# Performance work log

Hardware: AMD Instinct MI355X
Metric: run time of the kernel (lower is better)

Reference implementation:

```python
import jax, jax.numpy as jnp
import numpy as np

B = 16384          # batch_size
NF = 50            # n_fields
K = 16             # embedding_dim
V = 1_000_000      # input_dim (vocab)
H = 400            # fc hidden
NNZ = B * NF


def _xavier(key, shape):
    fan_in, fan_out = shape
    lim = (6.0 / (fan_in + fan_out)) ** 0.5
    return jax.random.uniform(key, shape, minval=-lim, maxval=lim, dtype=jnp.float32)


def setup_inputs() -> dict:
    key = jax.random.key(0)
    ks = jax.random.split(key, 12)
    feats = jax.random.randint(ks[0], (NNZ,), 0, V)
    # n_fields contiguous features per sample (required by view(batch_size,-1))
    index = jnp.repeat(jnp.arange(B), NF)
    values = jax.random.uniform(ks[1], (NNZ,), dtype=jnp.float32)
    bias = jnp.zeros((1, 1), jnp.float32)
    weights = _xavier(ks[2], (V, 1))
    embedding = _xavier(ks[3], (V, K))
    d = NF * K  # 800
    W0 = _xavier(ks[4], (d, H))
    b0 = jax.random.normal(ks[5], (1, 1), jnp.float32)
    W1 = _xavier(ks[6], (H, H))
    b1 = jax.random.normal(ks[7], (1, 1), jnp.float32)
    W2 = _xavier(ks[8], (H, 1))
    b2 = jax.random.normal(ks[9], (1, 1), jnp.float32)
    return dict(index=index, feats=feats, values=values, bias=bias,
                weights=weights, embedding=embedding,
                W0=W0, b0=b0, W1=W1, b1=b1, W2=W2, b2=b2, batch_size=B)


def reference(index, feats, values, bias, weights, embedding,
              W0, b0, W1, b1, W2, b2, batch_size):
    # gather (F.embedding)
    w = weights[feats, 0]              # [nnz]
    emb = embedding[feats]             # [nnz, K]

    # first order: segment-sum of w*v, plus bias ([B] + [1,1] -> [1,B], as in torch)
    first = jax.ops.segment_sum(w * values, index, num_segments=batch_size) + bias

    # second order: FM pooling trick, fused over all K dims in one segment reduce
    ev = emb * values[:, None]                                        # [nnz, K]
    s1 = jax.ops.segment_sum(ev, index, num_segments=batch_size)      # [B, K]
    s2 = jax.ops.segment_sum(ev * ev, index, num_segments=batch_size) # [B, K]
    second = 0.5 * jnp.sum(s1 * s1 - s2, axis=1)                      # [B]

    # higher order MLP (relu on every layer, scalar biases)
    x = emb.reshape(batch_size, -1)    # [B, NF*K]
    x = jax.nn.relu(x @ W0 + b0)
    x = jax.nn.relu(x @ W1 + b1)
    x = jax.nn.relu(x @ W2 + b2)       # [B, 1]
    higher = x.reshape(-1)             # [B]

    return jax.nn.sigmoid(first + second + higher)  # [1, B]
```

## Files before the change

### kernel.cpp

```cpp
#include <hip/hip_runtime.h>
#include <hip/hip_bf16.h>


#define BATCH 16384
#define NFLD  50
#define EK    16
#define DDIM  800
#define HDIM  400
#define HPAD  416
#define NPAD  512

#define TB_W0 400
#define TB_W1 208
#define TBLK  (TB_W0 + TB_W1)
#define GBLK  (BATCH / 16)

#define MROWS 64
#define NCOLS 448
#define WCOLS 112
#define NFRAG 7
#define P1    (DDIM / 32)
#define P2    (HPAD / 32)
#define H0S   424
#define NCHUNK (NCOLS / 16)

typedef __attribute__((ext_vector_type(8))) __bf16 bf16x8;
typedef __attribute__((ext_vector_type(4))) float  f32x4;

typedef const __attribute__((address_space(1))) unsigned int* gas_u32p;
typedef __attribute__((address_space(3))) unsigned int*       las_u32p;

__device__ __forceinline__ void gld_lds16(const void* g, void* l) {
    __builtin_amdgcn_global_load_lds((gas_u32p)g, (las_u32p)l, 16, 0, 0);
}

__global__ __launch_bounds__(256) void prep_kernel(
    const float* __restrict__ W0, const float* __restrict__ W1,
    __hip_bfloat16* __restrict__ W0t, __hip_bfloat16* __restrict__ W1t,
    const int* __restrict__ feats, const float* __restrict__ values,
    const float* __restrict__ biasp, const float* __restrict__ weights,
    const float* __restrict__ embedding,
    float* __restrict__ fs, __hip_bfloat16* __restrict__ x)
{
    const int bid = blockIdx.x;
    if (bid < TBLK) {
        const int which = bid >= TB_W0;
        const int i  = which ? bid - TB_W0 : bid;
        const int nx = which ? 13 : 25;
        const int bx = i % nx, by = i / nx;
        const float* src = which ? W1 : W0;
        __hip_bfloat16* dst = which ? W1t : W0t;
        const int srcK = which ? HDIM : DDIM;
        const int dstCols = which ? HPAD : DDIM;

        __shared__ float tile[32][33];
        const int tx = threadIdx.x & 31, ty = threadIdx.x >> 5;
        const int k0 = bx * 32, n0 = by * 32;
#pragma unroll
        for (int r = 0; r < 4; ++r) {
            int k = k0 + ty + r * 8;
            int n = n0 + tx;
            float v = (k < srcK && n < HDIM) ? src[(long)k * HDIM + n] : 0.f;
            tile[ty + r * 8][tx] = v;
        }
        __syncthreads();
#pragma unroll
        for (int r = 0; r < 4; ++r) {
            int n = n0 + ty + r * 8;
            int k = k0 + tx;
            if (k < dstCols)
                dst[(long)n * dstCols + k] = __float2bfloat16(tile[tx][ty + r * 8]);
        }
        return;
    }

    const int wave = threadIdx.x >> 6;
    const int lane = threadIdx.x & 63;
    const int r    = lane >> 2, c = lane & 3;
    const int sbase = (bid - TBLK) * 16 + wave * 4;

    int   f[4] = {0, 0, 0, 0};
    float v[4] = {0.f, 0.f, 0.f, 0.f};
    float wsum[4] = {0.f, 0.f, 0.f, 0.f};
#pragma unroll
    for (int q = 0; q < 4; ++q) {
        const long base = (long)(sbase + q) * NFLD;
        if (lane < NFLD) {
            f[q] = feats[base + lane];
            v[q] = values[base + lane];
            wsum[q] = weights[f[q]] * v[q];
        }
    }

    int   fj[4][4]; float vj[4][4];
#pragma unroll
    for (int q = 0; q < 4; ++q)
#pragma unroll
        for (int p = 0; p < 4; ++p) {
            const int j = p * 16 + r;
            if (p < 3 || r < 2) {
                fj[q][p] = __shfl(f[q], j);
                vj[q][p] = __shfl(v[q], j);
            }
        }
    float4 e[4][4];
#pragma unroll
    for (int q = 0; q < 4; ++q)
#pragma unroll
        for (int p = 0; p < 4; ++p)
            if (p < 3 || r < 2)
                e[q][p] = *(const float4*)(embedding + (long)fj[q][p] * EK + c * 4);

#pragma unroll
    for (int q = 0; q < 4; ++q) {
        const int s = sbase + q;
        f32x4 s1 = {0.f, 0.f, 0.f, 0.f}, s2 = {0.f, 0.f, 0.f, 0.f};
#pragma unroll
        for (int p = 0; p < 4; ++p) {
            const int j = p * 16 + r;
            if (p < 3 || r < 2) {
                f32x4 ef = {e[q][p].x, e[q][p].y, e[q][p].z, e[q][p].w};
                f32x4 ev = ef * vj[q][p];
                s1 += ev;
                s2 += ev * ev;
                __hip_bfloat16 pk[4] = {
                    __float2bfloat16(e[q][p].x), __float2bfloat16(e[q][p].y),
                    __float2bfloat16(e[q][p].z), __float2bfloat16(e[q][p].w)};
                *(uint2*)&x[(long)s * DDIM + j * EK + c * 4] = *(uint2*)pk;
            }
        }
#pragma unroll
        for (int m = 4; m <= 32; m <<= 1) {
            s1.x += __shfl_xor(s1.x, m); s1.y += __shfl_xor(s1.y, m);
            s1.z += __shfl_xor(s1.z, m); s1.w += __shfl_xor(s1.w, m);
            s2.x += __shfl_xor(s2.x, m); s2.y += __shfl_xor(s2.y, m);
            s2.z += __shfl_xor(s2.z, m); s2.w += __shfl_xor(s2.w, m);
        }
        float t = (s1.x * s1.x - s2.x) + (s1.y * s1.y - s2.y)
                + (s1.z * s1.z - s2.z) + (s1.w * s1.w - s2.w);
        t += __shfl_xor(t, 1); t += __shfl_xor(t, 2);
        float w = wsum[q];
        w += __shfl_xor(w, 1);  w += __shfl_xor(w, 2);
        w += __shfl_xor(w, 4);  w += __shfl_xor(w, 8);
        w += __shfl_xor(w, 16); w += __shfl_xor(w, 32);
        if (lane == 0) fs[s] = w + 0.5f * t + biasp[0];
    }
}

__global__ __launch_bounds__(512, 2) void fused_mlp_kernel(
    const __hip_bfloat16* __restrict__ x,
    const __hip_bfloat16* __restrict__ W0t, const __hip_bfloat16* __restrict__ W1t,
    const float* __restrict__ b0p, const float* __restrict__ b1p,
    const float* __restrict__ W2, const float* __restrict__ b2p,
    const float* __restrict__ fs, float* __restrict__ out)
{
    __shared__ __align__(16) __hip_bfloat16 sA[2][MROWS * 32];
    __shared__ __align__(16) __hip_bfloat16 sB[2][NCOLS * 32];
    __shared__ __align__(16) __hip_bfloat16 h0p[MROWS * H0S];
    __shared__ float red[MROWS][4];

    const int tid  = threadIdx.x;
    const int wave = tid >> 6, lane = tid & 63;
    const int l16  = lane & 15, quad = lane >> 4;
    const int waveM = wave & 1, waveN = wave >> 1;
    const int m0 = blockIdx.x * MROWS;
    const int rlane = lane >> 2, clane = (lane & 3) * 8;

    const float b0 = b0p[0];
    const float b1 = b1p[0];

    auto stage1 = [&](int p, int h) {
        const int k0 = p * 32;
#pragma unroll
        for (int c = 0; c < 4; ++c) {
            const int idx = wave * 4 + c;
            if (idx < 4) {
                gld_lds16(x + (long)(m0 + idx * 16 + rlane) * DDIM + k0 + clane,
                          &sA[h][idx * 512 + lane * 8]);
            } else {
                const int ch = idx - 4;
                gld_lds16(W0t + (long)(ch * 16 + rlane) * DDIM + k0 + clane,
                          &sB[h][ch * 512 + lane * 8]);
            }
        }
    };
    auto stage2 = [&](int p, int h) {
        const int k0 = p * 32;
#pragma unroll
        for (int c = 0; c < 4; ++c) {
            const int ch = wave + c * 8;
            if (ch < NCHUNK) {
                gld_lds16(W1t + (long)(ch * 16 + rlane) * HPAD + k0 + clane,
                          &sB[h][ch * 512 + lane * 8]);
            }
        }
    };

    f32x4 acc[2][NFRAG] = {};
    auto compute1 = [&](int h) {
        bf16x8 af[2], bfr[NFRAG];
#pragma unroll
        for (int i = 0; i < 2; ++i)
            af[i] = *(const bf16x8*)&sA[h][(waveM * 32 + i * 16 + l16) * 32 + quad * 8];
#pragma unroll
        for (int j = 0; j < NFRAG; ++j)
            bfr[j] = *(const bf16x8*)&sB[h][(waveN * WCOLS + j * 16 + l16) * 32 + quad * 8];
#pragma unroll
        for (int i = 0; i < 2; ++i)
#pragma unroll
            for (int j = 0; j < NFRAG; ++j)
                acc[i][j] = __builtin_amdgcn_mfma_f32_16x16x32_bf16(
                    af[i], bfr[j], acc[i][j], 0, 0, 0);
    };

    for (int kt = 0; kt + 1 < P1; kt += 2) {
        stage1(kt, 0); stage1(kt + 1, 1);
        __syncthreads();
        compute1(0); compute1(1);
        __syncthreads();
    }
    stage1(P1 - 1, 0);
    __syncthreads();
    compute1(0);
    __syncthreads();

#pragma unroll
    for (int i = 0; i < 2; ++i)
#pragma unroll
        for (int j = 0; j < NFRAG; ++j) {
            const int col = waveN * WCOLS + j * 16 + l16;
            if (col < HPAD) {
#pragma unroll
                for (int r = 0; r < 4; ++r) {
                    const int row = waveM * 32 + i * 16 + quad * 4 + r;
                    float v = acc[i][j][r] + b0;
                    v = v > 0.f ? v : 0.f;
                    if (col >= HDIM) v = 0.f;
                    h0p[row * H0S + col] = __float2bfloat16(v);
                }
            }
        }

    f32x4 acc2[2][NFRAG] = {};
    float w2v[NFRAG];
#pragma unroll
    for (int j = 0; j < NFRAG; ++j) {
        const int col = waveN * WCOLS + j * 16 + l16;
        w2v[j] = (col < HDIM) ? W2[col] : 0.f;
    }
    auto compute2 = [&](int h, int p) {
        bf16x8 af[2], bfr[NFRAG];
#pragma unroll
        for (int i = 0; i < 2; ++i)
            af[i] = *(const bf16x8*)&h0p[(waveM * 32 + i * 16 + l16) * H0S + p * 32 + quad * 8];
#pragma unroll
        for (int j = 0; j < NFRAG; ++j)
            bfr[j] = *(const bf16x8*)&sB[h][(waveN * WCOLS + j * 16 + l16) * 32 + quad * 8];
#pragma unroll
        for (int i = 0; i < 2; ++i)
#pragma unroll
            for (int j = 0; j < NFRAG; ++j)
                acc2[i][j] = __builtin_amdgcn_mfma_f32_16x16x32_bf16(
                    af[i], bfr[j], acc2[i][j], 0, 0, 0);
    };

    for (int kt = 0; kt + 1 < P2; kt += 2) {
        stage2(kt, 0); stage2(kt + 1, 1);
        __syncthreads();
        compute2(0, kt); compute2(1, kt + 1);
        __syncthreads();
    }
    stage2(P2 - 1, 0);
    __syncthreads();
    compute2(0, P2 - 1);

#pragma unroll
    for (int i = 0; i < 2; ++i)
#pragma unroll
        for (int r = 0; r < 4; ++r) {
            float ps = 0.f;
#pragma unroll
            for (int j = 0; j < NFRAG; ++j) {
                float v = acc2[i][j][r] + b1;
                v = v > 0.f ? v : 0.f;
                ps += v * w2v[j];
            }
            ps += __shfl_xor(ps, 1); ps += __shfl_xor(ps, 2);
            ps += __shfl_xor(ps, 4); ps += __shfl_xor(ps, 8);
            if (l16 == 0)
                red[waveM * 32 + i * 16 + quad * 4 + r][waveN] = ps;
        }
    __syncthreads();

    if (tid < MROWS) {
        const float s = (red[tid][0] + red[tid][1]) + (red[tid][2] + red[tid][3]);
        float hv = s + b2p[0];
        hv = hv > 0.f ? hv : 0.f;
        const float z = fs[m0 + tid] + hv;
        out[m0 + tid] = 1.f / (1.f + __expf(-z));
    }
}

extern "C" void kernel_launch(void* const* d_in, const int* in_sizes, int n_in,
                              void* d_out, int out_size, void* d_ws, size_t ws_size,
                              hipStream_t stream)
{
    const int*   feats     = (const int*)d_in[1];
    const float* values    = (const float*)d_in[2];
    const float* bias      = (const float*)d_in[3];
    const float* weights   = (const float*)d_in[4];
    const float* embedding = (const float*)d_in[5];
    const float* W0 = (const float*)d_in[6];
    const float* b0 = (const float*)d_in[7];
    const float* W1 = (const float*)d_in[8];
    const float* b1 = (const float*)d_in[9];
    const float* W2 = (const float*)d_in[10];
    const float* b2 = (const float*)d_in[11];

    char* ws = (char*)d_ws;
    size_t off = 0;
    auto alloc = [&](size_t bytes) {
        void* p = ws + off;
        off += (bytes + 255) & ~(size_t)255;
        return p;
    };
    float*          fs   = (float*)alloc((size_t)BATCH * 4);
    __hip_bfloat16* x    = (__hip_bfloat16*)alloc((size_t)BATCH * DDIM * 2);
    __hip_bfloat16* W0t  = (__hip_bfloat16*)alloc((size_t)NPAD * DDIM * 2);
    __hip_bfloat16* W1t  = (__hip_bfloat16*)alloc((size_t)NPAD * HPAD * 2);
    (void)ws_size; (void)in_sizes; (void)n_in; (void)out_size;

    prep_kernel<<<dim3(TBLK + GBLK), 256, 0, stream>>>(
        W0, W1, W0t, W1t, feats, values, bias, weights, embedding, fs, x);
    fused_mlp_kernel<<<dim3(BATCH / MROWS), 512, 0, stream>>>(
        x, W0t, W1t, b0, b1, W2, b2, fs, (float*)d_out);
}
```

Measured before the change: 181.1 us.

## Triple-buffer MLP GEMM staging with vmcnt waits, XOR swizzle and setprio

Replaces the double-buffered stage/compute loops of both MLP GEMMs with a three-stage ring buffer. Loads for step p+2 are issued before computing step p, and partial s_waitcnt vmcnt counts let the next loads stay in flight. The LDS tile layout gains an XOR swizzle on the K-chunk index to cut bank conflicts on fragment reads, and MFMA sections get raised wave priority. Because the LDS footprint grows, occupancy at two blocks per CU could suffer, and the hand-written vmcnt counts must exactly match the number of loads issued per wave.

```diff
diff --git a/kernel.cpp b/kernel.cpp
--- a/kernel.cpp
+++ b/kernel.cpp
@@ -22,7 +22,10 @@
 #define P1    (DDIM / 32)
 #define P2    (HPAD / 32)
 #define H0S   424
-#define NCHUNK (NCOLS / 16)
+#define SBUF  16384
+#define SBUF2 14336
+
+#define VMCNT(N) asm volatile("s_waitcnt vmcnt(" #N ")" ::: "memory")
 
 typedef __attribute__((ext_vector_type(8))) __bf16 bf16x8;
 typedef __attribute__((ext_vector_type(4))) float  f32x4;
@@ -32,6 +35,12 @@
 
 __device__ __forceinline__ void gld_lds16(const void* g, void* l) {
     __builtin_amdgcn_global_load_lds((gas_u32p)g, (las_u32p)l, 16, 0, 0);
+}
+
+__device__ __forceinline__ void bar() {
+    __builtin_amdgcn_sched_barrier(0);
+    __builtin_amdgcn_s_barrier();
+    __builtin_amdgcn_sched_barrier(0);
 }
 
 __global__ __launch_bounds__(256) void prep_kernel(
@@ -154,8 +163,7 @@
     const float* __restrict__ W2, const float* __restrict__ b2p,
     const float* __restrict__ fs, float* __restrict__ out)
 {
-    __shared__ __align__(16) __hip_bfloat16 sA[2][MROWS * 32];
-    __shared__ __align__(16) __hip_bfloat16 sB[2][NCOLS * 32];
+    __shared__ __align__(16) __hip_bfloat16 sS[3 * SBUF];
     __shared__ __align__(16) __hip_bfloat16 h0p[MROWS * H0S];
     __shared__ float red[MROWS][4];
 
@@ -164,65 +172,58 @@
     const int l16  = lane & 15, quad = lane >> 4;
     const int waveM = wave & 1, waveN = wave >> 1;
     const int m0 = blockIdx.x * MROWS;
-    const int rlane = lane >> 2, clane = (lane & 3) * 8;
+
+    const int rl  = lane >> 2;
+    const int swc = ((lane & 3) ^ ((lane >> 3) & 3)) * 8;
+    const int qsw = (quad ^ ((l16 >> 1) & 3)) * 8;
 
     const float b0 = b0p[0];
     const float b1 = b1p[0];
 
-    auto stage1 = [&](int p, int h) {
+    auto stage1 = [&](int p, int b) {
         const int k0 = p * 32;
+        __hip_bfloat16* dst = sS + b * SBUF;
 #pragma unroll
         for (int c = 0; c < 4; ++c) {
             const int idx = wave * 4 + c;
-            if (idx < 4) {
-                gld_lds16(x + (long)(m0 + idx * 16 + rlane) * DDIM + k0 + clane,
-                          &sA[h][idx * 512 + lane * 8]);
-            } else {
-                const int ch = idx - 4;
-                gld_lds16(W0t + (long)(ch * 16 + rlane) * DDIM + k0 + clane,
-                          &sB[h][ch * 512 + lane * 8]);
-            }
-        }
-    };
-    auto stage2 = [&](int p, int h) {
-        const int k0 = p * 32;
-#pragma unroll
-        for (int c = 0; c < 4; ++c) {
-            const int ch = wave + c * 8;
-            if (ch < NCHUNK) {
-                gld_lds16(W1t + (long)(ch * 16 + rlane) * HPAD + k0 + clane,
-                          &sB[h][ch * 512 + lane * 8]);
-            }
+            const __hip_bfloat16* src = (idx < 4)
+                ? x   + (long)(m0 + idx * 16 + rl) * DDIM + k0 + swc
+                : W0t + (long)((idx - 4) * 16 + rl) * DDIM + k0 + swc;
+            gld_lds16(src, dst + idx * 512 + lane * 8);
         }
     };
 
     f32x4 acc[2][NFRAG] = {};
-    auto compute1 = [&](int h) {
+    auto compute1 = [&](int b) {
+        const __hip_bfloat16* s = sS + b * SBUF;
         bf16x8 af[2], bfr[NFRAG];
 #pragma unroll
         for (int i = 0; i < 2; ++i)
-            af[i] = *(const bf16x8*)&sA[h][(waveM * 32 + i * 16 + l16) * 32 + quad * 8];
+            af[i] = *(const bf16x8*)&s[(waveM * 2 + i) * 512 + l16 * 32 + qsw];
 #pragma unroll
         for (int j = 0; j < NFRAG; ++j)
-            bfr[j] = *(const bf16x8*)&sB[h][(waveN * WCOLS + j * 16 + l16) * 32 + quad * 8];
+            bfr[j] = *(const bf16x8*)&s[(4 + waveN * NFRAG + j) * 512 + l16 * 32 + qsw];
+        __builtin_amdgcn_s_setprio(1);
 #pragma unroll
         for (int i = 0; i < 2; ++i)
 #pragma unroll
             for (int j = 0; j < NFRAG; ++j)
                 acc[i][j] = __builtin_amdgcn_mfma_f32_16x16x32_bf16(
                     af[i], bfr[j], acc[i][j], 0, 0, 0);
-    };
-
-    for (int kt = 0; kt + 1 < P1; kt += 2) {
-        stage1(kt, 0); stage1(kt + 1, 1);
-        __syncthreads();
-        compute1(0); compute1(1);
-        __syncthreads();
-    }
-    stage1(P1 - 1, 0);
-    __syncthreads();
-    compute1(0);
-    __syncthreads();
+        __builtin_amdgcn_s_setprio(0);
+    };
+
+    stage1(0, 0);
+    stage1(1, 1);
+    for (int p = 0; p < P1; ++p) {
+        if (p + 2 < P1) stage1(p + 2, (p + 2) % 3);
+        if      (p + 2 < P1) { VMCNT(8); }
+        else if (p + 1 < P1) { VMCNT(4); }
+        else                 { VMCNT(0); }
+        bar();
+        compute1(p % 3);
+        bar();
+    }
 
 #pragma unroll
     for (int i = 0; i < 2; ++i)
@@ -241,6 +242,18 @@
             }
         }
 
+    auto stage2 = [&](int p, int b) {
+        if (wave < 7) {
+            const int k0 = p * 32;
+#pragma unroll
+            for (int c = 0; c < 4; ++c) {
+                const int ch = wave * 4 + c;
+                gld_lds16(W1t + (long)(ch * 16 + rl) * HPAD + k0 + swc,
+                          sS + b * SBUF2 + ch * 512 + lane * 8);
+            }
+        }
+    };
+
     f32x4 acc2[2][NFRAG] = {};
     float w2v[NFRAG];
 #pragma unroll
@@ -248,31 +261,39 @@
         const int col = waveN * WCOLS + j * 16 + l16;
         w2v[j] = (col < HDIM) ? W2[col] : 0.f;
     }
-    auto compute2 = [&](int h, int p) {
+    auto compute2 = [&](int p, int b) {
+        const __hip_bfloat16* s = sS + b * SBUF2;
         bf16x8 af[2], bfr[NFRAG];
 #pragma unroll
         for (int i = 0; i < 2; ++i)
             af[i] = *(const bf16x8*)&h0p[(waveM * 32 + i * 16 + l16) * H0S + p * 32 + quad * 8];
 #pragma unroll
         for (int j = 0; j < NFRAG; ++j)
-            bfr[j] = *(const bf16x8*)&sB[h][(waveN * WCOLS + j * 16 + l16) * 32 + quad * 8];
+            bfr[j] = *(const bf16x8*)&s[(waveN * NFRAG + j) * 512 + l16 * 32 + qsw];
+        __builtin_amdgcn_s_setprio(1);
 #pragma unroll
         for (int i = 0; i < 2; ++i)
 #pragma unroll
             for (int j = 0; j < NFRAG; ++j)
                 acc2[i][j] = __builtin_amdgcn_mfma_f32_16x16x32_bf16(
                     af[i], bfr[j], acc2[i][j], 0, 0, 0);
-    };
-
-    for (int kt = 0; kt + 1 < P2; kt += 2) {
-        stage2(kt, 0); stage2(kt + 1, 1);
-        __syncthreads();
-        compute2(0, kt); compute2(1, kt + 1);
-        __syncthreads();
-    }
-    stage2(P2 - 1, 0);
-    __syncthreads();
-    compute2(0, P2 - 1);
+        __builtin_amdgcn_s_setprio(0);
+    };
+
+    stage2(0, 0);
+    stage2(1, 1);
+    asm volatile("s_waitcnt lgkmcnt(0)" ::: "memory");
+    bar();
+
+    for (int p = 0; p < P2; ++p) {
+        if (p + 2 < P2) stage2(p + 2, (p + 2) % 3);
+        if      (p + 2 < P2) { VMCNT(8); }
+        else if (p + 1 < P2) { VMCNT(4); }
+        else                 { VMCNT(0); }
+        bar();
+        compute2(p, p % 3);
+        bar();
+    }
 
 #pragma unroll
     for (int i = 0; i < 2; ++i)
```

After: 178.1 us. Within noise of the previous version (-1.7%).
